# Optimization experiments

Hardware: AMD Instinct MI355X
Metric: run time of the kernel (lower is better)

## Reference

```python
import jax, jax.numpy as jnp
import numpy as np

N_NODES = 65536
N_EDGES = 1048576
IN_FEATS = 128
N_HIDDEN = 64
N_LAYERS = 2
EPS = 1e-12  # matches torch F.normalize default eps


def setup_inputs() -> dict:
    key = jax.random.key(0)
    ks = jax.random.split(key, 8)
    features = jax.random.normal(ks[0], (N_NODES, IN_FEATS), dtype=jnp.float32)
    src = jax.random.randint(ks[1], (N_EDGES,), 0, N_NODES)
    dst = jax.random.randint(ks[2], (N_EDGES,), 0, N_NODES)
    W1 = jax.random.normal(ks[3], (IN_FEATS, N_HIDDEN), dtype=jnp.float32) * (1.0 / np.sqrt(IN_FEATS))
    b1 = jax.random.normal(ks[4], (N_HIDDEN,), dtype=jnp.float32) * 0.01
    W2 = jax.random.normal(ks[5], (N_HIDDEN, N_HIDDEN), dtype=jnp.float32) * (1.0 / np.sqrt(N_HIDDEN))
    b2 = jax.random.normal(ks[6], (N_HIDDEN,), dtype=jnp.float32) * 0.01
    betas = jnp.ones((N_LAYERS,), dtype=jnp.float32)  # init_beta=1, learnable
    return {"features": features, "src": src, "dst": dst,
            "W1": W1, "b1": b1, "W2": W2, "b2": b2, "betas": betas}


def agnn_conv(h, src, dst, beta, n_nodes):
    # L2-normalize node features (F.normalize, p=2)
    norm = jnp.sqrt(jnp.sum(h * h, axis=-1, keepdims=True))
    nh = h / jnp.maximum(norm, EPS)
    # cosine similarity along each edge: e_ij = beta * <nh_src, nh_dst>
    cos = jnp.sum(nh[src] * nh[dst], axis=-1)          # [E]
    e = beta * cos
    # edge softmax over incoming edges of each dst node (numerically stable)
    m = jax.ops.segment_max(e, dst, num_segments=n_nodes)   # [N], -inf for 0-in-degree
    ex = jnp.exp(e - m[dst])                                 # [E]
    s = jax.ops.segment_sum(ex, dst, num_segments=n_nodes)   # [N]
    alpha = ex / s[dst]                                      # [E]
    # weighted aggregation of UN-normalized source features
    out = jax.ops.segment_sum(alpha[:, None] * h[src], dst, num_segments=n_nodes)
    return out


def reference(features, src, dst, W1, b1, W2, b2, betas):
    h = jax.nn.relu(features @ W1 + b1)        # proj: Linear + ReLU
    for i in range(N_LAYERS):                   # stacked AGNNConv layers
        h = agnn_conv(h, src, dst, betas[i], N_NODES)
    return h @ W2 + b2                          # cls: Linear
```

## Files before the change

kernel.cpp:

```cpp
#include <hip/hip_runtime.h>

#define N_NODES 65536
#define N_EDGES 1048576
#define IN_FEATS 128
#define N_HIDDEN 64
#define PAD 64

static constexpr float F_EPS = 1e-12f;

__global__ __launch_bounds__(256) void scatter_pad_k(const int* __restrict__ src,
                                                     const int* __restrict__ dst,
                                                     int* __restrict__ deg,
                                                     int* __restrict__ csr) {
  int i = blockIdx.x * 256 + threadIdx.x;
  int d = dst[i];
  int s = src[i];
  int p = atomicAdd(&deg[d], 1);
  if (p < PAD) csr[(d << 6) + p] = s;
}

template <int K, bool RELU, bool RN>
__global__ __launch_bounds__(256) void gemm64_k(const float* __restrict__ A,
                                                const float* __restrict__ W,
                                                const float* __restrict__ bias,
                                                float* __restrict__ C,
                                                float* __restrict__ rn) {
  __shared__ float Wl[K * 64];
  int tid = threadIdx.x;
  {
    const float4* W4 = reinterpret_cast<const float4*>(W);
    float4* Wl4 = reinterpret_cast<float4*>(Wl);
    for (int i = tid; i < K * 16; i += 256) Wl4[i] = W4[i];
  }
  int lane = tid & 63;
  int wave = tid >> 6;
  float bv = bias[lane];
  int r0 = blockIdx.x * 64 + wave * 16;

  float a[16][K / 64];
#pragma unroll
  for (int r = 0; r < 16; ++r)
#pragma unroll
    for (int c = 0; c < K / 64; ++c)
      a[r][c] = A[(size_t)(r0 + r) * K + c * 64 + lane];

  float acc[16];
#pragma unroll
  for (int r = 0; r < 16; ++r) acc[r] = bv;

  __syncthreads();

#pragma unroll
  for (int c = 0; c < K / 64; ++c) {
#pragma unroll 8
    for (int kk = 0; kk < 64; ++kk) {
      float w = Wl[(c * 64 + kk) * 64 + lane];
#pragma unroll
      for (int r = 0; r < 16; ++r) {
        float av = __uint_as_float(
            __builtin_amdgcn_readlane(__float_as_uint(a[r][c]), kk));
        acc[r] = fmaf(av, w, acc[r]);
      }
    }
  }

#pragma unroll
  for (int r = 0; r < 16; ++r) {
    float v = acc[r];
    if (RELU) v = fmaxf(v, 0.0f);
    C[(size_t)(r0 + r) * 64 + lane] = v;
    if (RN) {
      float ss = v * v;
#pragma unroll
      for (int off = 32; off > 0; off >>= 1) ss += __shfl_xor(ss, off, 64);
      if (lane == 0) rn[r0 + r] = 1.0f / fmaxf(sqrtf(ss), F_EPS);
    }
  }
}

__global__ __launch_bounds__(256) void agnn_k(const float* __restrict__ X,
                                              const float* __restrict__ rn,
                                              const int* __restrict__ deg,
                                              const int* __restrict__ csr,
                                              const float* __restrict__ betas, int layer,
                                              float* __restrict__ Y,
                                              float* __restrict__ rn_out) {
  int node = blockIdx.x * 4 + (threadIdx.x >> 6);
  int lane = threadIdx.x & 63;
  int sl = lane & 15;
  int g = lane >> 4;
  float beta = betas[layer];

  const float4* X4 = reinterpret_cast<const float4*>(X);
  float4 hd = X4[(size_t)node * 16 + sl];
  float rnd = rn[node] * beta;
  int d = deg[node];
  int base = node << 6;

  float ssum = 0.0f;
  float4 acc = make_float4(0.f, 0.f, 0.f, 0.f);

  bool act0 = (g < d);
  int s0 = act0 ? csr[base + g] : node;
  float4 hs0 = X4[(size_t)s0 * 16 + sl];
  float rs0 = rn[s0];

  for (int i = 0; i < d; i += 4) {
    int e1 = i + 4 + g;
    bool act1 = (e1 < d);
    int s1 = act1 ? csr[base + e1] : node;
    float4 hs1 = X4[(size_t)s1 * 16 + sl];
    float rs1 = rn[s1];

    float p = hd.x * hs0.x;
    p = fmaf(hd.y, hs0.y, p);
    p = fmaf(hd.z, hs0.z, p);
    p = fmaf(hd.w, hs0.w, p);
#pragma unroll
    for (int off = 8; off > 0; off >>= 1) p += __shfl_xor(p, off, 64);
    float ex = act0 ? __expf(p * rnd * rs0) : 0.0f;
    ssum += ex;
    acc.x = fmaf(ex, hs0.x, acc.x);
    acc.y = fmaf(ex, hs0.y, acc.y);
    acc.z = fmaf(ex, hs0.z, acc.z);
    acc.w = fmaf(ex, hs0.w, acc.w);

    hs0 = hs1;
    rs0 = rs1;
    act0 = act1;
  }

#pragma unroll
  for (int off = 16; off < 64; off <<= 1) {
    ssum += __shfl_xor(ssum, off, 64);
    acc.x += __shfl_xor(acc.x, off, 64);
    acc.y += __shfl_xor(acc.y, off, 64);
    acc.z += __shfl_xor(acc.z, off, 64);
    acc.w += __shfl_xor(acc.w, off, 64);
  }

  float inv = (ssum > 0.0f) ? (1.0f / ssum) : 0.0f;
  float4 outv = make_float4(acc.x * inv, acc.y * inv, acc.z * inv, acc.w * inv);

  if (g == 0) {
    float4* Y4 = reinterpret_cast<float4*>(Y);
    Y4[(size_t)node * 16 + sl] = outv;
  }

  float ss = outv.x * outv.x + outv.y * outv.y + outv.z * outv.z + outv.w * outv.w;
#pragma unroll
  for (int off = 8; off > 0; off >>= 1) ss += __shfl_xor(ss, off, 64);
  if (lane == 0) rn_out[node] = 1.0f / fmaxf(sqrtf(ss), F_EPS);
}

extern "C" void kernel_launch(void* const* d_in, const int* in_sizes, int n_in,
                              void* d_out, int out_size, void* d_ws, size_t ws_size,
                              hipStream_t stream) {
  const float* features = (const float*)d_in[0];
  const int* src = (const int*)d_in[1];
  const int* dst = (const int*)d_in[2];
  const float* W1 = (const float*)d_in[3];
  const float* b1 = (const float*)d_in[4];
  const float* W2 = (const float*)d_in[5];
  const float* b2 = (const float*)d_in[6];
  const float* betas = (const float*)d_in[7];
  float* out = (float*)d_out;

  char* ws = (char*)d_ws;
  size_t off = 0;
  auto alloc = [&](size_t bytes) {
    void* p = ws + off;
    off += (bytes + 255) & ~255UL;
    return p;
  };
  float* hA = (float*)alloc((size_t)N_NODES * 64 * 4);
  float* hB = (float*)alloc((size_t)N_NODES * 64 * 4);
  float* rnA = (float*)alloc((size_t)N_NODES * 4);
  float* rnB = (float*)alloc((size_t)N_NODES * 4);
  int* deg = (int*)alloc((size_t)N_NODES * 4);
  int* csr = (int*)alloc((size_t)N_NODES * PAD * 4);

  hipMemsetAsync(deg, 0, (size_t)N_NODES * 4, stream);
  scatter_pad_k<<<N_EDGES / 256, 256, 0, stream>>>(src, dst, deg, csr);

  gemm64_k<IN_FEATS, true, true><<<N_NODES / 64, 256, 0, stream>>>(features, W1, b1, hA, rnA);

  agnn_k<<<N_NODES / 4, 256, 0, stream>>>(hA, rnA, deg, csr, betas, 0, hB, rnB);

  agnn_k<<<N_NODES / 4, 256, 0, stream>>>(hB, rnB, deg, csr, betas, 1, hA, rnA);

  gemm64_k<N_HIDDEN, false, false><<<N_NODES / 64, 256, 0, stream>>>(hA, W2, b2, out, nullptr);
}
```

Before: 318.5 us.

## Fuse edge scatter with input projection and widen AGNN edge parallelism

Merges the CSR scatter kernel and the first projection GEMM into one launch, with odd blocks doing vectorized int4 edge scatter and even blocks doing the GEMM, so the two independent stages overlap. The GEMM now stages W in 64-row chunks to cut shared memory to 16KB. The AGNN kernel processes 8 edges per wave at a time, with each lane handling 8 features via two float4s, so fewer shuffle steps are needed per edge. This adds more register pressure, and the mixed block roles may imbalance the work across blocks.

```diff
diff --git a/kernel.cpp b/kernel.cpp
--- a/kernel.cpp
+++ b/kernel.cpp
@@ -8,15 +8,88 @@
 
 static constexpr float F_EPS = 1e-12f;
 
-__global__ __launch_bounds__(256) void scatter_pad_k(const int* __restrict__ src,
-                                                     const int* __restrict__ dst,
-                                                     int* __restrict__ deg,
-                                                     int* __restrict__ csr) {
-  int i = blockIdx.x * 256 + threadIdx.x;
-  int d = dst[i];
-  int s = src[i];
-  int p = atomicAdd(&deg[d], 1);
-  if (p < PAD) csr[(d << 6) + p] = s;
+template <int K, bool RELU, bool RN>
+__device__ __forceinline__ void gemm_body(const float* __restrict__ A,
+                                          const float* __restrict__ W,
+                                          const float* __restrict__ bias,
+                                          float* __restrict__ C,
+                                          float* __restrict__ rn,
+                                          int block64, int tid, float* Wl) {
+  int lane = tid & 63;
+  int wave = tid >> 6;
+  float bv = bias[lane];
+  int r0 = block64 * 64 + wave * 16;
+
+  float a[16][K / 64];
+#pragma unroll
+  for (int r = 0; r < 16; ++r)
+#pragma unroll
+    for (int c = 0; c < K / 64; ++c)
+      a[r][c] = A[(size_t)(r0 + r) * K + c * 64 + lane];
+
+  float acc[16];
+#pragma unroll
+  for (int r = 0; r < 16; ++r) acc[r] = bv;
+
+  const float4* W4 = reinterpret_cast<const float4*>(W);
+  float4* Wl4 = reinterpret_cast<float4*>(Wl);
+
+#pragma unroll
+  for (int c = 0; c < K / 64; ++c) {
+    __syncthreads();
+#pragma unroll
+    for (int i = tid; i < 64 * 16; i += 256) Wl4[i] = W4[c * 64 * 16 + i];
+    __syncthreads();
+#pragma unroll 8
+    for (int kk = 0; kk < 64; ++kk) {
+      float w = Wl[kk * 64 + lane];
+#pragma unroll
+      for (int r = 0; r < 16; ++r) {
+        float av = __uint_as_float(
+            __builtin_amdgcn_readlane(__float_as_uint(a[r][c]), kk));
+        acc[r] = fmaf(av, w, acc[r]);
+      }
+    }
+  }
+
+#pragma unroll
+  for (int r = 0; r < 16; ++r) {
+    float v = acc[r];
+    if (RELU) v = fmaxf(v, 0.0f);
+    C[(size_t)(r0 + r) * 64 + lane] = v;
+    if (RN) {
+      float ss = v * v;
+#pragma unroll
+      for (int off = 32; off > 0; off >>= 1) ss += __shfl_xor(ss, off, 64);
+      if (lane == 0) rn[r0 + r] = 1.0f / fmaxf(sqrtf(ss), F_EPS);
+    }
+  }
+}
+
+__global__ __launch_bounds__(256) void proj_scatter_k(
+    const float* __restrict__ A, const float* __restrict__ W,
+    const float* __restrict__ bias, float* __restrict__ C, float* __restrict__ rn,
+    const int* __restrict__ src, const int* __restrict__ dst,
+    int* __restrict__ deg, int* __restrict__ csr) {
+  __shared__ float Wl[64 * 64];
+  int bb = blockIdx.x;
+  if (bb & 1) {
+    int t = (bb >> 1) * 256 + threadIdx.x;
+    const int4* s4 = reinterpret_cast<const int4*>(src);
+    const int4* d4 = reinterpret_cast<const int4*>(dst);
+    int4 sv = s4[t];
+    int4 dv = d4[t];
+    int p0 = atomicAdd(&deg[dv.x], 1);
+    int p1 = atomicAdd(&deg[dv.y], 1);
+    int p2 = atomicAdd(&deg[dv.z], 1);
+    int p3 = atomicAdd(&deg[dv.w], 1);
+    if (p0 < PAD) csr[(dv.x << 6) + p0] = sv.x;
+    if (p1 < PAD) csr[(dv.y << 6) + p1] = sv.y;
+    if (p2 < PAD) csr[(dv.z << 6) + p2] = sv.z;
+    if (p3 < PAD) csr[(dv.w << 6) + p3] = sv.w;
+  } else {
+    gemm_body<IN_FEATS, true, true>(A, W, bias, C, rn, bb >> 1, threadIdx.x, Wl);
+  }
 }
 
 template <int K, bool RELU, bool RN>
@@ -25,57 +98,8 @@
                                                 const float* __restrict__ bias,
                                                 float* __restrict__ C,
                                                 float* __restrict__ rn) {
-  __shared__ float Wl[K * 64];
-  int tid = threadIdx.x;
-  {
-    const float4* W4 = reinterpret_cast<const float4*>(W);
-    float4* Wl4 = reinterpret_cast<float4*>(Wl);
-    for (int i = tid; i < K * 16; i += 256) Wl4[i] = W4[i];
-  }
-  int lane = tid & 63;
-  int wave = tid >> 6;
-  float bv = bias[lane];
-  int r0 = blockIdx.x * 64 + wave * 16;
-
-  float a[16][K / 64];
-#pragma unroll
-  for (int r = 0; r < 16; ++r)
-#pragma unroll
-    for (int c = 0; c < K / 64; ++c)
-      a[r][c] = A[(size_t)(r0 + r) * K + c * 64 + lane];
-
-  float acc[16];
-#pragma unroll
-  for (int r = 0; r < 16; ++r) acc[r] = bv;
-
-  __syncthreads();
-
-#pragma unroll
-  for (int c = 0; c < K / 64; ++c) {
-#pragma unroll 8
-    for (int kk = 0; kk < 64; ++kk) {
-      float w = Wl[(c * 64 + kk) * 64 + lane];
-#pragma unroll
-      for (int r = 0; r < 16; ++r) {
-        float av = __uint_as_float(
-            __builtin_amdgcn_readlane(__float_as_uint(a[r][c]), kk));
-        acc[r] = fmaf(av, w, acc[r]);
-      }
-    }
-  }
-
-#pragma unroll
-  for (int r = 0; r < 16; ++r) {
-    float v = acc[r];
-    if (RELU) v = fmaxf(v, 0.0f);
-    C[(size_t)(r0 + r) * 64 + lane] = v;
-    if (RN) {
-      float ss = v * v;
-#pragma unroll
-      for (int off = 32; off > 0; off >>= 1) ss += __shfl_xor(ss, off, 64);
-      if (lane == 0) rn[r0 + r] = 1.0f / fmaxf(sqrtf(ss), F_EPS);
-    }
-  }
+  __shared__ float Wl[64 * 64];
+  gemm_body<K, RELU, RN>(A, W, bias, C, rn, blockIdx.x, threadIdx.x, Wl);
 }
 
 __global__ __launch_bounds__(256) void agnn_k(const float* __restrict__ X,
@@ -87,69 +111,87 @@
                                               float* __restrict__ rn_out) {
   int node = blockIdx.x * 4 + (threadIdx.x >> 6);
   int lane = threadIdx.x & 63;
-  int sl = lane & 15;
-  int g = lane >> 4;
+  int sl = lane & 7;
+  int g = lane >> 3;
   float beta = betas[layer];
 
   const float4* X4 = reinterpret_cast<const float4*>(X);
-  float4 hd = X4[(size_t)node * 16 + sl];
+  float4 hd0 = X4[(size_t)node * 16 + sl * 2];
+  float4 hd1 = X4[(size_t)node * 16 + sl * 2 + 1];
   float rnd = rn[node] * beta;
   int d = deg[node];
   int base = node << 6;
 
   float ssum = 0.0f;
-  float4 acc = make_float4(0.f, 0.f, 0.f, 0.f);
+  float4 acc0 = make_float4(0.f, 0.f, 0.f, 0.f);
+  float4 acc1 = make_float4(0.f, 0.f, 0.f, 0.f);
 
   bool act0 = (g < d);
   int s0 = act0 ? csr[base + g] : node;
-  float4 hs0 = X4[(size_t)s0 * 16 + sl];
+  float4 hs0a = X4[(size_t)s0 * 16 + sl * 2];
+  float4 hs0b = X4[(size_t)s0 * 16 + sl * 2 + 1];
   float rs0 = rn[s0];
 
-  for (int i = 0; i < d; i += 4) {
-    int e1 = i + 4 + g;
+  for (int i = 0; i < d; i += 8) {
+    int e1 = i + 8 + g;
     bool act1 = (e1 < d);
     int s1 = act1 ? csr[base + e1] : node;
-    float4 hs1 = X4[(size_t)s1 * 16 + sl];
+    float4 hs1a = X4[(size_t)s1 * 16 + sl * 2];
+    float4 hs1b = X4[(size_t)s1 * 16 + sl * 2 + 1];
     float rs1 = rn[s1];
 
-    float p = hd.x * hs0.x;
-    p = fmaf(hd.y, hs0.y, p);
-    p = fmaf(hd.z, hs0.z, p);
-    p = fmaf(hd.w, hs0.w, p);
-#pragma unroll
-    for (int off = 8; off > 0; off >>= 1) p += __shfl_xor(p, off, 64);
+    float pa = hd0.x * hs0a.x;
+    pa = fmaf(hd0.y, hs0a.y, pa);
+    pa = fmaf(hd0.z, hs0a.z, pa);
+    pa = fmaf(hd0.w, hs0a.w, pa);
+    float pb = hd1.x * hs0b.x;
+    pb = fmaf(hd1.y, hs0b.y, pb);
+    pb = fmaf(hd1.z, hs0b.z, pb);
+    pb = fmaf(hd1.w, hs0b.w, pb);
+    float p = pa + pb;
+#pragma unroll
+    for (int off = 4; off > 0; off >>= 1) p += __shfl_xor(p, off, 64);
     float ex = act0 ? __expf(p * rnd * rs0) : 0.0f;
     ssum += ex;
-    acc.x = fmaf(ex, hs0.x, acc.x);
-    acc.y = fmaf(ex, hs0.y, acc.y);
-    acc.z = fmaf(ex, hs0.z, acc.z);
-    acc.w = fmaf(ex, hs0.w, acc.w);
-
-    hs0 = hs1;
-    rs0 = rs1;
-    act0 = act1;
-  }
-
-#pragma unroll
-  for (int off = 16; off < 64; off <<= 1) {
+    acc0.x = fmaf(ex, hs0a.x, acc0.x);
+    acc0.y = fmaf(ex, hs0a.y, acc0.y);
+    acc0.z = fmaf(ex, hs0a.z, acc0.z);
+    acc0.w = fmaf(ex, hs0a.w, acc0.w);
+    acc1.x = fmaf(ex, hs0b.x, acc1.x);
+    acc1.y = fmaf(ex, hs0b.y, acc1.y);
+    acc1.z = fmaf(ex, hs0b.z, acc1.z);
+    acc1.w = fmaf(ex, hs0b.w, acc1.w);
+
+    hs0a = hs1a; hs0b = hs1b; rs0 = rs1; act0 = act1;
+  }
+
+#pragma unroll
+  for (int off = 8; off < 64; off <<= 1) {
     ssum += __shfl_xor(ssum, off, 64);
-    acc.x += __shfl_xor(acc.x, off, 64);
-    acc.y += __shfl_xor(acc.y, off, 64);
-    acc.z += __shfl_xor(acc.z, off, 64);
-    acc.w += __shfl_xor(acc.w, off, 64);
+    acc0.x += __shfl_xor(acc0.x, off, 64);
+    acc0.y += __shfl_xor(acc0.y, off, 64);
+    acc0.z += __shfl_xor(acc0.z, off, 64);
+    acc0.w += __shfl_xor(acc0.w, off, 64);
+    acc1.x += __shfl_xor(acc1.x, off, 64);
+    acc1.y += __shfl_xor(acc1.y, off, 64);
+    acc1.z += __shfl_xor(acc1.z, off, 64);
+    acc1.w += __shfl_xor(acc1.w, off, 64);
   }
 
   float inv = (ssum > 0.0f) ? (1.0f / ssum) : 0.0f;
-  float4 outv = make_float4(acc.x * inv, acc.y * inv, acc.z * inv, acc.w * inv);
+  float4 out0 = make_float4(acc0.x * inv, acc0.y * inv, acc0.z * inv, acc0.w * inv);
+  float4 out1 = make_float4(acc1.x * inv, acc1.y * inv, acc1.z * inv, acc1.w * inv);
 
   if (g == 0) {
     float4* Y4 = reinterpret_cast<float4*>(Y);
-    Y4[(size_t)node * 16 + sl] = outv;
-  }
-
-  float ss = outv.x * outv.x + outv.y * outv.y + outv.z * outv.z + outv.w * outv.w;
-#pragma unroll
-  for (int off = 8; off > 0; off >>= 1) ss += __shfl_xor(ss, off, 64);
+    Y4[(size_t)node * 16 + sl * 2] = out0;
+    Y4[(size_t)node * 16 + sl * 2 + 1] = out1;
+  }
+
+  float ss = out0.x * out0.x + out0.y * out0.y + out0.z * out0.z + out0.w * out0.w;
+  ss += out1.x * out1.x + out1.y * out1.y + out1.z * out1.z + out1.w * out1.w;
+#pragma unroll
+  for (int off = 4; off > 0; off >>= 1) ss += __shfl_xor(ss, off, 64);
   if (lane == 0) rn_out[node] = 1.0f / fmaxf(sqrtf(ss), F_EPS);
 }
 
@@ -181,9 +223,9 @@
   int* csr = (int*)alloc((size_t)N_NODES * PAD * 4);
 
   hipMemsetAsync(deg, 0, (size_t)N_NODES * 4, stream);
-  scatter_pad_k<<<N_EDGES / 256, 256, 0, stream>>>(src, dst, deg, csr);
-
-  gemm64_k<IN_FEATS, true, true><<<N_NODES / 64, 256, 0, stream>>>(features, W1, b1, hA, rnA);
+
+  proj_scatter_k<<<2048, 256, 0, stream>>>(features, W1, b1, hA, rnA,
+                                           src, dst, deg, csr);
 
   agnn_k<<<N_NODES / 4, 256, 0, stream>>>(hA, rnA, deg, csr, betas, 0, hB, rnB);
 
```

Result: faster. 283.9 us (-10.9%).
